# Performance work log

Hardware: AMD Instinct MI355X
Metric: run time of the kernel (lower is better)

The kernel has to match this reference:

```python
import jax, jax.numpy as jnp
import numpy as np

B, N, C = 2, 2048, 1024
H = 16
HD = C // H  # 64


def setup_inputs() -> dict:
    key = jax.random.key(0)
    k1, k2, k3 = jax.random.split(key, 3)
    x = jax.random.normal(k1, (B, N, C), dtype=jnp.float32)
    w_qkv = jax.random.normal(k2, (C, 3 * C), dtype=jnp.float32) * (C ** -0.5)
    b_qkv = jnp.zeros((3 * C,), dtype=jnp.float32)
    w_out = jax.random.normal(k3, (C, C), dtype=jnp.float32) * (C ** -0.5)
    b_out = jnp.zeros((C,), dtype=jnp.float32)
    return {"x": x, "w_qkv": w_qkv, "b_qkv": b_qkv, "w_out": w_out, "b_out": b_out}


def reference(x, w_qkv, b_qkv, w_out, b_out):
    scale = HD ** -0.5
    # QKV projection: (B,N,3C) -> (B,N,3,H,HD) -> (B,3,H,N,HD)
    qkv = (jnp.einsum('bnc,cd->bnd', x, w_qkv) + b_qkv)
    qkv = qkv.reshape(B, N, 3, H, HD).transpose(0, 2, 3, 1, 4)
    q, k, v = qkv[:, 0], qkv[:, 1], qkv[:, 2]  # each (B,H,N,HD)
    # scaled dot-product attention with full NxN matrix (as in source)
    attn = jnp.einsum('bhnd,bhmd->bhnm', q, k) * scale
    attn = jax.nn.softmax(attn, axis=-1)
    out = jnp.einsum('bhnm,bhmd->bhnd', attn, v)  # (B,H,N,HD)
    out = out.transpose(0, 2, 1, 3).reshape(B, N, C)
    out = jnp.einsum('bnc,cd->bnd', out, w_out) + b_out
    return out
```

## Files before the change

### kernel.cpp

```cpp
#include <hip/hip_runtime.h>
#include <stdint.h>

using uint = unsigned int;
using ushort = unsigned short;

constexpr int Bb = 2;
constexpr int Ns = 2048;
constexpr int Cd = 1024;
constexpr int Hh = 16;
constexpr int HD = 64;
constexpr int BHND = Bb * Hh * Ns * HD;

typedef __attribute__((ext_vector_type(8))) short short8;
typedef __attribute__((ext_vector_type(4))) float floatx4;

__device__ inline ushort f2bf(float f) {
  uint u = __float_as_uint(f);
  return (ushort)((u + 0x7fffu + ((u >> 16) & 1u)) >> 16);
}
__device__ inline ushort f2bfr(float f) {
  return (ushort)((__float_as_uint(f) + 0x8000u) >> 16);
}

__global__ __launch_bounds__(256) void cvt_f32_bf16(
    const float* __restrict__ in, ushort* __restrict__ outp) {
  const int i = blockIdx.x * 256 + threadIdx.x;
  const float4 v = ((const float4*)in)[i];
  ushort4 o;
  o.x = f2bf(v.x); o.y = f2bf(v.y); o.z = f2bf(v.z); o.w = f2bf(v.w);
  ((ushort4*)outp)[i] = o;
}

__global__ __launch_bounds__(256) void transpose_f32_bf16(
    const float* __restrict__ in, ushort* __restrict__ outp, int R, int Cc) {
  __shared__ alignas(16) ushort tile[32][33];
  const int c0 = blockIdx.x * 32, r0 = blockIdx.y * 32;
  const int tx = threadIdx.x & 31;
  const int ty = threadIdx.x >> 5;
#pragma unroll
  for (int i = 0; i < 4; ++i)
    tile[ty + 8 * i][tx] = f2bf(in[(size_t)(r0 + ty + 8 * i) * Cc + c0 + tx]);
  __syncthreads();
#pragma unroll
  for (int i = 0; i < 4; ++i)
    outp[(size_t)(c0 + ty + 8 * i) * R + r0 + tx] = tile[tx][ty + 8 * i];
}

template <int MODE>
__global__ __launch_bounds__(256) void gemm_bt(
    const ushort* __restrict__ A, const ushort* __restrict__ Bt,
    const float* __restrict__ bias, void* __restrict__ outp,
    int M, int K, int Nn) {
  constexpr int LDT = 40;
  __shared__ alignas(16) ushort As[128 * LDT];
  __shared__ alignas(16) ushort Bs[128 * LDT];
  const int tid = threadIdx.x;
  const int wave = tid >> 6, lane = tid & 63;
  const int quad = lane >> 4, l16 = lane & 15;
  const int wr = wave >> 1, wc = wave & 1;
  const int m0 = blockIdx.x * 128, n0 = blockIdx.y * 128;

  const int srow0 = tid >> 2;
  const int skc = (tid & 3) * 8;

  const ushort* pa = A + (size_t)(m0 + srow0) * K + skc;
  const ushort* pb = Bt + (size_t)(n0 + srow0) * K + skc;

  floatx4 acc[4][4];
#pragma unroll
  for (int i = 0; i < 4; ++i)
#pragma unroll
    for (int j = 0; j < 4; ++j) {
      acc[i][j][0] = 0.f; acc[i][j][1] = 0.f; acc[i][j][2] = 0.f; acc[i][j][3] = 0.f;
    }

  uint4 ra0 = *(const uint4*)(pa);
  uint4 ra1 = *(const uint4*)(pa + (size_t)64 * K);
  uint4 rb0 = *(const uint4*)(pb);
  uint4 rb1 = *(const uint4*)(pb + (size_t)64 * K);

  const int nkt = K >> 5;
  for (int kt = 0; kt < nkt; ++kt) {
    __syncthreads();
    *(uint4*)&As[srow0 * LDT + skc] = ra0;
    *(uint4*)&As[(srow0 + 64) * LDT + skc] = ra1;
    *(uint4*)&Bs[srow0 * LDT + skc] = rb0;
    *(uint4*)&Bs[(srow0 + 64) * LDT + skc] = rb1;
    __syncthreads();
    if (kt + 1 < nkt) {
      const ushort* qa = pa + (size_t)(kt + 1) * 32;
      const ushort* qb = pb + (size_t)(kt + 1) * 32;
      ra0 = *(const uint4*)(qa);
      ra1 = *(const uint4*)(qa + (size_t)64 * K);
      rb0 = *(const uint4*)(qb);
      rb1 = *(const uint4*)(qb + (size_t)64 * K);
    }
    short8 af[4], bfv[4];
#pragma unroll
    for (int mt = 0; mt < 4; ++mt)
      af[mt] = *(const short8*)&As[(wr * 64 + mt * 16 + l16) * LDT + quad * 8];
#pragma unroll
    for (int nt = 0; nt < 4; ++nt)
      bfv[nt] = *(const short8*)&Bs[(wc * 64 + nt * 16 + l16) * LDT + quad * 8];
#pragma unroll
    for (int mt = 0; mt < 4; ++mt)
#pragma unroll
      for (int nt = 0; nt < 4; ++nt)
        acc[mt][nt] = __builtin_amdgcn_mfma_f32_16x16x32_bf16(af[mt], bfv[nt],
                                                              acc[mt][nt], 0, 0, 0);
  }

  if (MODE == 0) {
    ushort* qp = (ushort*)outp;
    ushort* kp = qp + BHND;
    ushort* vp = qp + 2 * BHND;
#pragma unroll
    for (int nt = 0; nt < 4; ++nt) {
      const int gn = n0 + wc * 64 + nt * 16 + l16;
      const float bv = bias[gn];
      const int which = gn >> 10, cc = gn & 1023;
      const int h = cc >> 6, d = cc & 63;
#pragma unroll
      for (int mt = 0; mt < 4; ++mt) {
#pragma unroll
        for (int r = 0; r < 4; ++r) {
          const int gm = m0 + wr * 64 + mt * 16 + quad * 4 + r;
          const int b = gm >> 11, n = gm & 2047;
          const ushort o = f2bfr(acc[mt][nt][r] + bv);
          const int bh = b * Hh + h;
          if (which == 0)
            qp[((size_t)bh * Ns + n) * HD + d] = o;
          else if (which == 1)
            kp[((size_t)bh * Ns + n) * HD + d] = o;
          else
            vp[((size_t)bh * HD + d) * Ns + n] = o;
        }
      }
    }
  } else {
    float* fout = (float*)outp;
#pragma unroll
    for (int nt = 0; nt < 4; ++nt) {
      const int gn = n0 + wc * 64 + nt * 16 + l16;
      const float bv = bias[gn];
#pragma unroll
      for (int mt = 0; mt < 4; ++mt)
#pragma unroll
        for (int r = 0; r < 4; ++r) {
          const int gm = m0 + wr * 64 + mt * 16 + quad * 4 + r;
          fout[(size_t)gm * Nn + gn] = acc[mt][nt][r] + bv;
        }
    }
  }
}

__global__ __launch_bounds__(256, 2) void attn(
    const ushort* __restrict__ q, const ushort* __restrict__ k,
    const ushort* __restrict__ vT, ushort* __restrict__ aout) {
  constexpr int LDK = 72;
  __shared__ alignas(16) ushort Ks[64 * LDK];
  __shared__ alignas(16) ushort Vs[64 * LDK];
  const int tid = threadIdx.x;
  const int wave = tid >> 6, lane = tid & 63;
  const int quad = lane >> 4, l16 = lane & 15;
  const int bh = blockIdx.y;
  const int qw = blockIdx.x * 128 + wave * 32;

  const ushort* kb = k + (size_t)bh * Ns * HD;
  const ushort* vb = vT + (size_t)bh * HD * Ns;

  short8 aq[2][2];
#pragma unroll
  for (int nqi = 0; nqi < 2; ++nqi) {
    const ushort* qp = q + ((size_t)bh * Ns + qw + nqi * 16 + l16) * HD + quad * 8;
    aq[nqi][0] = *(const short8*)(qp);
    aq[nqi][1] = *(const short8*)(qp + 32);
  }

  floatx4 accO[4][2];
#pragma unroll
  for (int mt = 0; mt < 4; ++mt)
#pragma unroll
    for (int nqi = 0; nqi < 2; ++nqi) {
      accO[mt][nqi][0] = 0.f; accO[mt][nqi][1] = 0.f;
      accO[mt][nqi][2] = 0.f; accO[mt][nqi][3] = 0.f;
    }
  float lst[2] = {0.f, 0.f};

  const int srow = tid >> 2;
  const int g0 = (tid & 3) * 2;
  const int cbA = (g0 >> 2) * 8 + ((g0 >> 1) & 1);
  const int g1 = g0 + 1;
  const int cbB = (g1 >> 2) * 8 + 4 + ((g1 >> 1) & 1);

  const ushort* kgp = kb + (size_t)srow * HD + g0 * 8;
  const ushort* vgp = vb + (size_t)srow * Ns + g0 * 8;
  ushort* ksw = &Ks[srow * LDK + g0 * 8];
  ushort* vswA = &Vs[srow * LDK + cbA * 4];
  ushort* vswB = &Vs[srow * LDK + cbB * 4];

  uint4 kg0 = *(const uint4*)(kgp);
  uint4 kg1 = *(const uint4*)(kgp + 8);
  uint4 vg0 = *(const uint4*)(vgp);
  uint4 vg1 = *(const uint4*)(vgp + 8);

  for (int kv0 = 0; kv0 < Ns; kv0 += 64) {
    __syncthreads();
    *(uint4*)ksw = kg0;
    *(uint4*)(ksw + 8) = kg1;
    *(uint2*)vswA = make_uint2(vg0.x, vg0.y);
    *(uint2*)(vswA + 8) = make_uint2(vg0.z, vg0.w);
    *(uint2*)vswB = make_uint2(vg1.x, vg1.y);
    *(uint2*)(vswB + 8) = make_uint2(vg1.z, vg1.w);
    __syncthreads();

    short8 ak[4][2], av[4][2];
#pragma unroll
    for (int t4 = 0; t4 < 4; ++t4) {
      const int ro = (t4 * 16 + l16) * LDK + quad * 8;
      ak[t4][0] = *(const short8*)&Ks[ro];
      ak[t4][1] = *(const short8*)&Ks[ro + 32];
      av[t4][0] = *(const short8*)&Vs[ro];
      av[t4][1] = *(const short8*)&Vs[ro + 32];
    }
    if (kv0 + 64 < Ns) {
      kg0 = *(const uint4*)(kgp + (size_t)(kv0 + 64) * HD);
      kg1 = *(const uint4*)(kgp + (size_t)(kv0 + 64) * HD + 8);
      vg0 = *(const uint4*)(vgp + kv0 + 64);
      vg1 = *(const uint4*)(vgp + kv0 + 64 + 8);
    }

#pragma unroll
    for (int nqi = 0; nqi < 2; ++nqi) {
      floatx4 sacc[4];
#pragma unroll
      for (int kvt = 0; kvt < 4; ++kvt) {
        sacc[kvt][0] = 0.f; sacc[kvt][1] = 0.f;
        sacc[kvt][2] = 0.f; sacc[kvt][3] = 0.f;
      }
#pragma unroll
      for (int kd = 0; kd < 2; ++kd)
#pragma unroll
        for (int kvt = 0; kvt < 4; ++kvt)
          sacc[kvt] = __builtin_amdgcn_mfma_f32_16x16x32_bf16(
              ak[kvt][kd], aq[nqi][kd], sacc[kvt], 0, 0, 0);

      uint ul[4], uh[4];
      float ls = 0.f;
#pragma unroll
      for (int kvt = 0; kvt < 4; ++kvt) {
        const float p0 = exp2f(sacc[kvt][0] * 0.18033688f);
        const float p1 = exp2f(sacc[kvt][1] * 0.18033688f);
        const float p2 = exp2f(sacc[kvt][2] * 0.18033688f);
        const float p3 = exp2f(sacc[kvt][3] * 0.18033688f);
        ls += (p0 + p1) + (p2 + p3);
        ul[kvt] = __builtin_amdgcn_perm(__float_as_uint(p1) + 0x8000u,
                                        __float_as_uint(p0) + 0x8000u, 0x07060302u);
        uh[kvt] = __builtin_amdgcn_perm(__float_as_uint(p3) + 0x8000u,
                                        __float_as_uint(p2) + 0x8000u, 0x07060302u);
      }
      lst[nqi] += ls;

#pragma unroll
      for (int ks = 0; ks < 2; ++ks) {
        union { uint u[4]; short8 s; } pf;
        pf.u[0] = ul[2 * ks]; pf.u[1] = uh[2 * ks];
        pf.u[2] = ul[2 * ks + 1]; pf.u[3] = uh[2 * ks + 1];
#pragma unroll
        for (int mt = 0; mt < 4; ++mt)
          accO[mt][nqi] = __builtin_amdgcn_mfma_f32_16x16x32_bf16(
              av[mt][ks], pf.s, accO[mt][nqi], 0, 0, 0);
      }
    }
  }

  const int b = bh >> 4, h = bh & 15;
#pragma unroll
  for (int nqi = 0; nqi < 2; ++nqi) {
    float l = lst[nqi];
    l += __shfl_xor(l, 16, 64);
    l += __shfl_xor(l, 32, 64);
    const float inv = 1.f / l;
    const int n = qw + nqi * 16 + l16;
#pragma unroll
    for (int mt = 0; mt < 4; ++mt) {
      ushort4 o;
      o.x = f2bfr(accO[mt][nqi][0] * inv);
      o.y = f2bfr(accO[mt][nqi][1] * inv);
      o.z = f2bfr(accO[mt][nqi][2] * inv);
      o.w = f2bfr(accO[mt][nqi][3] * inv);
      *(ushort4*)&aout[((size_t)(b * Ns + n)) * Cd + h * HD + mt * 16 + quad * 4] = o;
    }
  }
}

extern "C" void kernel_launch(void* const* d_in, const int* in_sizes, int n_in,
                              void* d_out, int out_size, void* d_ws, size_t ws_size,
                              hipStream_t stream) {
  (void)in_sizes; (void)n_in; (void)out_size; (void)ws_size;
  const float* x = (const float*)d_in[0];
  const float* w_qkv = (const float*)d_in[1];
  const float* b_qkv = (const float*)d_in[2];
  const float* w_out = (const float*)d_in[3];
  const float* b_out = (const float*)d_in[4];

  ushort* xbf = (ushort*)d_ws;
  ushort* wqkvT = xbf + (size_t)BHND;
  ushort* woutT = wqkvT + 3072 * 1024;
  ushort* qkvbuf = woutT + 1024 * 1024;
  ushort* aout = qkvbuf + 3 * (size_t)BHND;

  cvt_f32_bf16<<<dim3(BHND / 1024), 256, 0, stream>>>(x, xbf);
  transpose_f32_bf16<<<dim3(96, 32), 256, 0, stream>>>(w_qkv, wqkvT, 1024, 3072);
  transpose_f32_bf16<<<dim3(32, 32), 256, 0, stream>>>(w_out, woutT, 1024, 1024);

  gemm_bt<0><<<dim3(32, 24), 256, 0, stream>>>(xbf, wqkvT, b_qkv, qkvbuf,
                                               4096, 1024, 3072);
  attn<<<dim3(16, 32), 256, 0, stream>>>(qkvbuf, qkvbuf + BHND,
                                         qkvbuf + 2 * (size_t)BHND, aout);
  gemm_bt<1><<<dim3(32, 8), 256, 0, stream>>>(aout, woutT, b_out, d_out,
                                              4096, 1024, 1024);
}
```

Measured before the change: 206.8 us.

## Fold softmax scale into Q projection, use native exp2 and packed bf16 conversion

Folds the softmax scale times log2(e) into the Q output of the QKV projection, which removes a multiply per score in the attention inner loop. It also switches to the raw hardware exp2 builtin, converts probabilities with the v_cvt_pk_bf16_f32 instruction instead of perm-based truncation, strength-reduces the prefetch addressing, and wraps the MFMA groups in s_setprio. Quantising Q after scaling slightly changes rounding, and the raw exp2 skips denormal and range handling. No max subtraction is done, so overflow is still possible, but that was already true before.

```diff
diff --git a/kernel.cpp b/kernel.cpp
--- a/kernel.cpp
+++ b/kernel.cpp
@@ -11,6 +11,8 @@
 constexpr int HD = 64;
 constexpr int BHND = Bb * Hh * Ns * HD;
 
+constexpr float QSCL = 0.18033688f;
+
 typedef __attribute__((ext_vector_type(8))) short short8;
 typedef __attribute__((ext_vector_type(4))) float floatx4;
 
@@ -20,6 +22,11 @@
 }
 __device__ inline ushort f2bfr(float f) {
   return (ushort)((__float_as_uint(f) + 0x8000u) >> 16);
+}
+__device__ inline uint cvt_pk_bf16(float lo, float hi) {
+  uint r;
+  asm("v_cvt_pk_bf16_f32 %0, %1, %2" : "=v"(r) : "v"(lo), "v"(hi));
+  return r;
 }
 
 __global__ __launch_bounds__(256) void cvt_f32_bf16(
@@ -120,13 +127,14 @@
       const float bv = bias[gn];
       const int which = gn >> 10, cc = gn & 1023;
       const int h = cc >> 6, d = cc & 63;
+      const float sc = (which == 0) ? QSCL : 1.0f;
 #pragma unroll
       for (int mt = 0; mt < 4; ++mt) {
 #pragma unroll
         for (int r = 0; r < 4; ++r) {
           const int gm = m0 + wr * 64 + mt * 16 + quad * 4 + r;
           const int b = gm >> 11, n = gm & 2047;
-          const ushort o = f2bfr(acc[mt][nt][r] + bv);
+          const ushort o = f2bfr((acc[mt][nt][r] + bv) * sc);
           const int bh = b * Hh + h;
           if (which == 0)
             qp[((size_t)bh * Ns + n) * HD + d] = o;
@@ -186,6 +194,7 @@
       accO[mt][nqi][2] = 0.f; accO[mt][nqi][3] = 0.f;
     }
   float lst[2] = {0.f, 0.f};
+  const floatx4 fz = {0.f, 0.f, 0.f, 0.f};
 
   const int srow = tid >> 2;
   const int g0 = (tid & 3) * 2;
@@ -203,6 +212,8 @@
   uint4 kg1 = *(const uint4*)(kgp + 8);
   uint4 vg0 = *(const uint4*)(vgp);
   uint4 vg1 = *(const uint4*)(vgp + 8);
+  const ushort* kpre = kgp + 64 * HD;
+  const ushort* vpre = vgp + 64;
 
   for (int kv0 = 0; kv0 < Ns; kv0 += 64) {
     __syncthreads();
@@ -224,53 +235,54 @@
       av[t4][1] = *(const short8*)&Vs[ro + 32];
     }
     if (kv0 + 64 < Ns) {
-      kg0 = *(const uint4*)(kgp + (size_t)(kv0 + 64) * HD);
-      kg1 = *(const uint4*)(kgp + (size_t)(kv0 + 64) * HD + 8);
-      vg0 = *(const uint4*)(vgp + kv0 + 64);
-      vg1 = *(const uint4*)(vgp + kv0 + 64 + 8);
+      kg0 = *(const uint4*)(kpre);
+      kg1 = *(const uint4*)(kpre + 8);
+      vg0 = *(const uint4*)(vpre);
+      vg1 = *(const uint4*)(vpre + 8);
+      kpre += 64 * HD;
+      vpre += 64;
     }
 
 #pragma unroll
     for (int nqi = 0; nqi < 2; ++nqi) {
       floatx4 sacc[4];
+      __builtin_amdgcn_s_setprio(1);
+#pragma unroll
+      for (int kvt = 0; kvt < 4; ++kvt)
+        sacc[kvt] = __builtin_amdgcn_mfma_f32_16x16x32_bf16(
+            ak[kvt][0], aq[nqi][0], fz, 0, 0, 0);
+#pragma unroll
+      for (int kvt = 0; kvt < 4; ++kvt)
+        sacc[kvt] = __builtin_amdgcn_mfma_f32_16x16x32_bf16(
+            ak[kvt][1], aq[nqi][1], sacc[kvt], 0, 0, 0);
+      __builtin_amdgcn_s_setprio(0);
+
+      uint pk[4][2];
+      float ls = 0.f;
 #pragma unroll
       for (int kvt = 0; kvt < 4; ++kvt) {
-        sacc[kvt][0] = 0.f; sacc[kvt][1] = 0.f;
-        sacc[kvt][2] = 0.f; sacc[kvt][3] = 0.f;
-      }
-#pragma unroll
-      for (int kd = 0; kd < 2; ++kd)
-#pragma unroll
-        for (int kvt = 0; kvt < 4; ++kvt)
-          sacc[kvt] = __builtin_amdgcn_mfma_f32_16x16x32_bf16(
-              ak[kvt][kd], aq[nqi][kd], sacc[kvt], 0, 0, 0);
-
-      uint ul[4], uh[4];
-      float ls = 0.f;
-#pragma unroll
-      for (int kvt = 0; kvt < 4; ++kvt) {
-        const float p0 = exp2f(sacc[kvt][0] * 0.18033688f);
-        const float p1 = exp2f(sacc[kvt][1] * 0.18033688f);
-        const float p2 = exp2f(sacc[kvt][2] * 0.18033688f);
-        const float p3 = exp2f(sacc[kvt][3] * 0.18033688f);
+        const float p0 = __builtin_amdgcn_exp2f(sacc[kvt][0]);
+        const float p1 = __builtin_amdgcn_exp2f(sacc[kvt][1]);
+        const float p2 = __builtin_amdgcn_exp2f(sacc[kvt][2]);
+        const float p3 = __builtin_amdgcn_exp2f(sacc[kvt][3]);
         ls += (p0 + p1) + (p2 + p3);
-        ul[kvt] = __builtin_amdgcn_perm(__float_as_uint(p1) + 0x8000u,
-                                        __float_as_uint(p0) + 0x8000u, 0x07060302u);
-        uh[kvt] = __builtin_amdgcn_perm(__float_as_uint(p3) + 0x8000u,
-                                        __float_as_uint(p2) + 0x8000u, 0x07060302u);
+        pk[kvt][0] = cvt_pk_bf16(p0, p1);
+        pk[kvt][1] = cvt_pk_bf16(p2, p3);
       }
       lst[nqi] += ls;
 
+      __builtin_amdgcn_s_setprio(1);
 #pragma unroll
       for (int ks = 0; ks < 2; ++ks) {
         union { uint u[4]; short8 s; } pf;
-        pf.u[0] = ul[2 * ks]; pf.u[1] = uh[2 * ks];
-        pf.u[2] = ul[2 * ks + 1]; pf.u[3] = uh[2 * ks + 1];
+        pf.u[0] = pk[2 * ks][0]; pf.u[1] = pk[2 * ks][1];
+        pf.u[2] = pk[2 * ks + 1][0]; pf.u[3] = pk[2 * ks + 1][1];
 #pragma unroll
         for (int mt = 0; mt < 4; ++mt)
           accO[mt][nqi] = __builtin_amdgcn_mfma_f32_16x16x32_bf16(
               av[mt][ks], pf.s, accO[mt][nqi], 0, 0, 0);
       }
+      __builtin_amdgcn_s_setprio(0);
     }
   }
 
```

Result: faster. 188.0 us (-9.1%).
